# Kernel tuning notes

Hardware: AMD Instinct MI355X
Metric: run time of the kernel (lower is better)

The kernel has to match this reference:

```python
import jax, jax.numpy as jnp
import numpy as np

B, D, S = 16384, 2048, 512      # batch, input_dim, sideinfo_dim
E, H1, H2 = 8, 1024, 512        # subexpert_num, subexpert_unit
EPS = 1e-5                       # BatchNorm eps (torch default)


def setup_inputs() -> dict:
    key = jax.random.key(0)
    ks = jax.random.split(key, 16)
    inp = {
        "input": jax.random.normal(ks[0], (B, D), jnp.float32),
        "sideinfo": jax.random.normal(ks[1], (B, S), jnp.float32),
        # expert layer 1: Linear(D->H1) per expert, batched over E
        "W1": jax.random.normal(ks[2], (E, D, H1), jnp.float32) / np.sqrt(D),
        "b1": jax.random.normal(ks[3], (E, H1), jnp.float32) * 0.01,
        "gamma1": 1.0 + 0.01 * jax.random.normal(ks[4], (E, H1), jnp.float32),
        "beta1": jax.random.normal(ks[5], (E, H1), jnp.float32) * 0.01,
        "mean1": jax.random.normal(ks[6], (E, H1), jnp.float32) * 0.01,
        "var1": jax.random.uniform(ks[7], (E, H1), jnp.float32, 0.5, 1.5),
        # expert layer 2: Linear(H1->H2) per expert
        "W2": jax.random.normal(ks[8], (E, H1, H2), jnp.float32) / np.sqrt(H1),
        "b2": jax.random.normal(ks[9], (E, H2), jnp.float32) * 0.01,
        "gamma2": 1.0 + 0.01 * jax.random.normal(ks[10], (E, H2), jnp.float32),
        "beta2": jax.random.normal(ks[11], (E, H2), jnp.float32) * 0.01,
        "mean2": jax.random.normal(ks[12], (E, H2), jnp.float32) * 0.01,
        "var2": jax.random.uniform(ks[13], (E, H2), jnp.float32, 0.5, 1.5),
        # gate: Linear(S->E) + softmax
        "Wg": jax.random.normal(ks[14], (S, E), jnp.float32) / np.sqrt(S),
        "bg": jax.random.normal(ks[15], (E,), jnp.float32) * 0.01,
    }
    return inp


def _bn(x, gamma, beta, mean, var):
    # eval-mode BatchNorm1d with per-expert running stats; x: [B,E,H]
    return (x - mean) * (gamma * jax.lax.rsqrt(var + EPS)) + beta


def reference(input, sideinfo, W1, b1, gamma1, beta1, mean1, var1,
              W2, b2, gamma2, beta2, mean2, var2, Wg, bg):
    # all E expert MLPs as two batched GEMMs (dropout is identity in eval)
    h = jnp.einsum('bd,edh->beh', input, W1) + b1            # [B,E,H1]
    h = jax.nn.relu(_bn(h, gamma1, beta1, mean1, var1))
    o = jnp.einsum('beh,eho->beo', h, W2) + b2               # [B,E,H2]
    o = jax.nn.relu(_bn(o, gamma2, beta2, mean2, var2))
    gate = jax.nn.softmax(sideinfo @ Wg + bg, axis=1)        # [B,E]
    return jnp.einsum('beo,be->bo', o, gate)                 # [B,H2]
```

## Files before the change

kernel.cpp:

```cpp
#include <hip/hip_runtime.h>
#include <hip/hip_bf16.h>

static constexpr int B_  = 16384;
static constexpr int D_  = 2048;
static constexpr int S_  = 512;
static constexpr int E_  = 8;
static constexpr int H1_ = 1024;
static constexpr int H2_ = 512;
static constexpr float EPS_ = 1e-5f;

typedef __bf16 bf16x8 __attribute__((ext_vector_type(8)));
typedef float  f32x4  __attribute__((ext_vector_type(4)));

static __device__ __forceinline__ unsigned short f2bf(float f) {
    unsigned u = __float_as_uint(f);
    unsigned r = (u + 0x7fffu + ((u >> 16) & 1u)) >> 16;
    return (unsigned short)r;
}


__global__ void cvt_bf16_kernel(const float* __restrict__ in, ushort* __restrict__ out, long n) {
    long i = ((long)blockIdx.x * blockDim.x + threadIdx.x) * 4;
    long stride = (long)gridDim.x * blockDim.x * 4;
    for (; i < n; i += stride) {
        float4 v = *(const float4*)(in + i);
        ushort4 o;
        o.x = f2bf(v.x); o.y = f2bf(v.y); o.z = f2bf(v.z); o.w = f2bf(v.w);
        *(ushort4*)(out + i) = o;
    }
}

__global__ void transpose_cvt_kernel(const float* __restrict__ in, ushort* __restrict__ out,
                                     int R, int C) {
    __shared__ float t[64][65];
    int nbr = R >> 6, nbc = C >> 6;
    int bid = blockIdx.x;
    int e = bid / (nbr * nbc);
    int rem = bid % (nbr * nbc);
    int br = (rem / nbc) << 6, bc = (rem % nbc) << 6;
    const float* ip = in + (size_t)e * R * C;
    ushort* op = out + (size_t)e * R * C;
    int tcol = (threadIdx.x & 15) * 4;
    int trow = threadIdx.x >> 4;
#pragma unroll
    for (int p = 0; p < 4; p++) {
        int r = trow + p * 16;
        float4 v = *(const float4*)(ip + (size_t)(br + r) * C + bc + tcol);
        t[r][tcol + 0] = v.x; t[r][tcol + 1] = v.y; t[r][tcol + 2] = v.z; t[r][tcol + 3] = v.w;
    }
    __syncthreads();
#pragma unroll
    for (int p = 0; p < 4; p++) {
        int c = trow + p * 16;
        ushort4 o;
        o.x = f2bf(t[tcol + 0][c]);
        o.y = f2bf(t[tcol + 1][c]);
        o.z = f2bf(t[tcol + 2][c]);
        o.w = f2bf(t[tcol + 3][c]);
        *(ushort4*)(op + (size_t)(bc + c) * R + br + tcol) = o;
    }
}

__global__ void fold_bn_kernel(const float* __restrict__ gamma, const float* __restrict__ beta,
                               const float* __restrict__ mean, const float* __restrict__ var,
                               const float* __restrict__ bias,
                               float* __restrict__ Sv, float* __restrict__ Tv, int n) {
    int i = blockIdx.x * 256 + threadIdx.x;
    if (i < n) {
        float s = gamma[i] * rsqrtf(var[i] + EPS_);
        Sv[i] = s;
        Tv[i] = (bias[i] - mean[i]) * s + beta[i];
    }
}

__global__ void gate_kernel(const float* __restrict__ side, const float* __restrict__ Wg,
                            const float* __restrict__ bg, float* __restrict__ gate) {
    int wid = threadIdx.x >> 6, lane = threadIdx.x & 63;
    int b = blockIdx.x * 4 + wid;
    const float* sp = side + (size_t)b * S_ + lane * 8;
    float4 v0 = *(const float4*)sp;
    float4 v1 = *(const float4*)(sp + 4);
    float sv[8] = {v0.x, v0.y, v0.z, v0.w, v1.x, v1.y, v1.z, v1.w};
    float acc[E_] = {0,0,0,0,0,0,0,0};
    const float* wrow = Wg + (size_t)(lane * 8) * E_;
#pragma unroll
    for (int j = 0; j < 8; j++) {
        float4 w0 = *(const float4*)(wrow + j * E_);
        float4 w1 = *(const float4*)(wrow + j * E_ + 4);
        acc[0] += sv[j] * w0.x; acc[1] += sv[j] * w0.y;
        acc[2] += sv[j] * w0.z; acc[3] += sv[j] * w0.w;
        acc[4] += sv[j] * w1.x; acc[5] += sv[j] * w1.y;
        acc[6] += sv[j] * w1.z; acc[7] += sv[j] * w1.w;
    }
#pragma unroll
    for (int off = 32; off; off >>= 1)
#pragma unroll
        for (int e = 0; e < E_; e++) acc[e] += __shfl_xor(acc[e], off, 64);
    float m = -1e30f;
#pragma unroll
    for (int e = 0; e < E_; e++) { acc[e] += bg[e]; m = fmaxf(m, acc[e]); }
    float s = 0.f;
#pragma unroll
    for (int e = 0; e < E_; e++) { acc[e] = __expf(acc[e] - m); s += acc[e]; }
    float inv = 1.f / s;
    if (lane < E_) gate[(size_t)b * E_ + lane] = acc[lane] * inv;
}


__device__ __forceinline__ void g2lds16(const void* g, void* l) {
    __builtin_amdgcn_global_load_lds((const __attribute__((address_space(1))) unsigned int*)g,
                                     (__attribute__((address_space(3))) unsigned int*)l,
                                     16, 0, 0);
}

#define BAR()      asm volatile("s_barrier" ::: "memory")
#define WAITVM(n)  asm volatile("s_waitcnt vmcnt(" #n ")" ::: "memory")
#define MFMA(a,b,c) __builtin_amdgcn_mfma_f32_16x16x32_bf16((a),(b),(c),0,0,0)


template<int EPI>
__global__ __launch_bounds__(512, 2)
void gemm8(const ushort* __restrict__ A, const ushort* __restrict__ Bt, long aBatch,
           const float* __restrict__ Sv, const float* __restrict__ Tv,
           ushort* __restrict__ hout, float* __restrict__ outp, const float* __restrict__ gate,
           int M, int N, int K, int tilesN, int tilesM)
{
    extern __shared__ char smem[];

    const int NT  = K >> 6;
    const int tpe = tilesM * tilesN;

    const int nwg = gridDim.x, per = nwg >> 3;
    const int b0  = blockIdx.x;
    const int bid = (b0 & 7) * per + (b0 >> 3);

    const int e   = bid / tpe;
    const int rem = bid % tpe;
    const int tm  = rem / tilesN, tn = rem % tilesN;

    const char* aBase = (const char*)(A + (size_t)e * aBatch + (size_t)tm * 256 * K);
    const char* bBase = (const char*)(Bt + (size_t)e * N * K + (size_t)tn * 256 * K);
    const size_t rowB = (size_t)K * 2;
    const size_t half2 = 64 * rowB;
    const size_t half1 = 128 * rowB;

    const int tid = threadIdx.x, w = tid >> 6, lane = tid & 63;
    const int wm = w >> 2, wn = w & 3;

    const int srow = tid >> 3;
    const int scol_sw = ((tid & 7) * 16) ^ ((srow & 7) << 4);
    const int ldsW = w * 1024;

    const int lr = lane & 15;
    const int cks0 = ((lane >> 4) * 16) ^ ((lane & 7) << 4);
    const int cks1 = (64 + (lane >> 4) * 16) ^ ((lane & 7) << 4);
    const char* rdA0 = smem + 65536 + (wm * 128 + lr) * 128 + cks0;
    const char* rdA1 = smem + 65536 + (wm * 128 + lr) * 128 + cks1;
    const char* rdB0 = smem + (wn * 64 + lr) * 128 + cks0;
    const char* rdB1 = smem + (wn * 64 + lr) * 128 + cks1;

#define STG(gp, ldsoff) do { \
        g2lds16((gp), smem + (ldsoff)); \
        g2lds16((gp) + half2, smem + (ldsoff) + 8192); } while (0)

    const char* ga = aBase + (size_t)srow * rowB + scol_sw;
    const char* gb = bBase + (size_t)srow * rowB + scol_sw;

    f32x4 acc[8][4] = {};
    bf16x8 aC[4], aN[4], bC[4], bN[4];

    STG(ga,         65536 + 0 + 0     + ldsW);
    STG(ga + half1, 65536 + 0 + 16384 + ldsW);
    STG(gb,         0     + 0 + 0     + ldsW);
    STG(gb + half1, 0     + 0 + 16384 + ldsW);
    WAITVM(0);
    BAR();

#pragma unroll
    for (int mf = 0; mf < 4; ++mf) aC[mf] = *(const bf16x8*)(rdA0 + mf * 2048);
#pragma unroll
    for (int nf = 0; nf < 4; ++nf) bC[nf] = *(const bf16x8*)(rdB0 + nf * 2048);

    const char* spA0 = ga + 128;
    const char* spA1 = ga + half1 + 128;
    const char* spB0 = gb + 128;
    const char* spB1 = gb + half1 + 128;

#pragma unroll 2
    for (int t = 0; t < NT; ++t) {
        const int bi   = t & 1;
        const int oR   = bi * 32768;
        const int oRN  = (bi ^ 1) * 32768;
        const int oSA  = 65536 + (bi ^ 1) * 32768;
        const int oSB  = (bi ^ 1) * 32768;
        const bool more = (t < NT - 1);

#pragma unroll
        for (int mf = 0; mf < 4; ++mf) aN[mf] = *(const bf16x8*)(rdA0 + oR + (4 + mf) * 2048);
        if (more) {
            STG(spA0, oSA + 0 + ldsW);
            STG(spA1, oSA + 16384 + ldsW);
        }
        __builtin_amdgcn_s_setprio(1);
#pragma unroll
        for (int mf = 0; mf < 4; ++mf)
#pragma unroll
            for (int nf = 0; nf < 4; ++nf)
                acc[mf][nf] = MFMA(aC[mf], bC[nf], acc[mf][nf]);
        __builtin_amdgcn_s_setprio(0);

#pragma unroll
        for (int mf = 0; mf < 4; ++mf) aC[mf] = *(const bf16x8*)(rdA1 + oR + mf * 2048);
#pragma unroll
        for (int nf = 0; nf < 4; ++nf) bN[nf] = *(const bf16x8*)(rdB1 + oR + nf * 2048);
        if (more) STG(spB0, oSB + 0 + ldsW);
        __builtin_amdgcn_s_setprio(1);
#pragma unroll
        for (int mf = 0; mf < 4; ++mf)
#pragma unroll
            for (int nf = 0; nf < 4; ++nf)
                acc[4 + mf][nf] = MFMA(aN[mf], bC[nf], acc[4 + mf][nf]);
        __builtin_amdgcn_s_setprio(0);

#pragma unroll
        for (int mf = 0; mf < 4; ++mf) aN[mf] = *(const bf16x8*)(rdA1 + oR + (4 + mf) * 2048);
        if (more) STG(spB1, oSB + 16384 + ldsW);
        __builtin_amdgcn_s_setprio(1);
#pragma unroll
        for (int mf = 0; mf < 4; ++mf)
#pragma unroll
            for (int nf = 0; nf < 4; ++nf)
                acc[mf][nf] = MFMA(aC[mf], bN[nf], acc[mf][nf]);
        __builtin_amdgcn_s_setprio(0);

        __builtin_amdgcn_s_setprio(1);
#pragma unroll
        for (int mf = 0; mf < 4; ++mf)
#pragma unroll
            for (int nf = 0; nf < 4; ++nf)
                acc[4 + mf][nf] = MFMA(aN[mf], bN[nf], acc[4 + mf][nf]);
        __builtin_amdgcn_s_setprio(0);

        if (more) {
            WAITVM(0);
            BAR();
#pragma unroll
            for (int mf = 0; mf < 4; ++mf) aC[mf] = *(const bf16x8*)(rdA0 + oRN + mf * 2048);
#pragma unroll
            for (int nf = 0; nf < 4; ++nf) bC[nf] = *(const bf16x8*)(rdB0 + oRN + nf * 2048);
        }

        spA0 += 128; spA1 += 128; spB0 += 128; spB1 += 128;
    }

    const int rbase = tm * 256 + wm * 128 + (lane >> 4) * 4;
    const int cbase = tn * 256 + wn * 64 + lr;
    if (EPI == 1) {
#pragma unroll
        for (int nf = 0; nf < 4; ++nf) {
            const int col = cbase + nf * 16;
            const float s = Sv[e * N + col];
            const float tt = Tv[e * N + col];
#pragma unroll
            for (int mf = 0; mf < 8; ++mf) {
                const int row0 = rbase + mf * 16;
                f32x4 v = acc[mf][nf];
#pragma unroll
                for (int r = 0; r < 4; ++r) {
                    float x = v[r] * s + tt;
                    x = x > 0.f ? x : 0.f;
                    hout[((size_t)e * M + row0 + r) * N + col] = f2bf(x);
                }
            }
        }
    }
#undef STG
}


__global__ __launch_bounds__(512, 2)
void gemm2e(const ushort* __restrict__ H, const ushort* __restrict__ W2T,
            const float* __restrict__ Sv, const float* __restrict__ Tv,
            const float* __restrict__ gate, float* __restrict__ outp)
{
    extern __shared__ char smem[];

    const int b0 = blockIdx.x;
    const int bid = (b0 & 7) * 32 + (b0 >> 3);
    const int tm = bid >> 1, tn = bid & 1;

    const size_t rowB  = (size_t)H1_ * 2;
    const size_t strAE = (size_t)B_ * H1_ * 2;
    const size_t strBE = (size_t)H2_ * H1_ * 2;
    const size_t half2 = 64 * rowB;
    const size_t halfB = 128 * rowB;

    const int tid = threadIdx.x, w = tid >> 6, lane = tid & 63;
    const int wm = w >> 2, wn = w & 3;

    const int srow = tid >> 3;
    const int scol_sw = ((tid & 7) * 16) ^ ((srow & 7) << 4);
    const int ldsW = w * 1024;

    const int lr = lane & 15;
    const int cks0 = ((lane >> 4) * 16) ^ ((lane & 7) << 4);
    const int cks1 = (64 + (lane >> 4) * 16) ^ ((lane & 7) << 4);
    const char* rdA0 = smem + 65536 + (wm * 64 + lr) * 128 + cks0;
    const char* rdA1 = smem + 65536 + (wm * 64 + lr) * 128 + cks1;
    const char* rdB0 = smem + (wn * 64 + lr) * 128 + cks0;
    const char* rdB1 = smem + (wn * 64 + lr) * 128 + cks1;

    const char* ga = (const char*)H + (size_t)tm * 128 * rowB + (size_t)srow * rowB + scol_sw;
    const char* gb = (const char*)W2T + (size_t)tn * 256 * rowB + (size_t)srow * rowB + scol_sw;

    f32x4 acc[4][4] = {};
    f32x4 oacc[4][4] = {};
    bf16x8 a0[4], a1[4], b0v[4], b1v[4];

    g2lds16(ga,                 smem + 65536 + 0     + ldsW);
    g2lds16(ga + half2,         smem + 65536 + 8192  + ldsW);
    g2lds16(gb,                 smem + 0     + ldsW);
    g2lds16(gb + half2,         smem + 8192  + ldsW);
    g2lds16(gb + halfB,         smem + 16384 + ldsW);
    g2lds16(gb + halfB + half2, smem + 24576 + ldsW);
    WAITVM(0);
    BAR();

#pragma unroll
    for (int mf = 0; mf < 4; ++mf) a0[mf] = *(const bf16x8*)(rdA0 + mf * 2048);
#pragma unroll
    for (int nf = 0; nf < 4; ++nf) b0v[nf] = *(const bf16x8*)(rdB0 + nf * 2048);

    const int rbase = tm * 128 + wm * 64 + (lane >> 4) * 4;
    const int cbase = tn * 256 + wn * 64 + lr;

#pragma unroll 2
    for (int t = 0; t < 128; ++t) {
        const int bi   = t & 1;
        const int oA   = bi * 16384;
        const int oB   = bi * 32768;
        const int oAn  = (bi ^ 1) * 16384;
        const int oBn  = (bi ^ 1) * 32768;
        const bool more = (t < 127);

        const int t1 = t + 1;
        const char* gA1 = ga + (size_t)(t1 >> 4) * strAE + (t1 & 15) * 128;
        const char* gB1 = gb + (size_t)(t1 >> 4) * strBE + (t1 & 15) * 128;

#pragma unroll
        for (int mf = 0; mf < 4; ++mf) a1[mf] = *(const bf16x8*)(rdA1 + oA + mf * 2048);
#pragma unroll
        for (int nf = 0; nf < 4; ++nf) b1v[nf] = *(const bf16x8*)(rdB1 + oB + nf * 2048);
        if (more) {
            g2lds16(gA1,         smem + 65536 + oAn + 0    + ldsW);
            g2lds16(gA1 + half2, smem + 65536 + oAn + 8192 + ldsW);
            g2lds16(gB1,         smem + oBn + 0    + ldsW);
            g2lds16(gB1 + half2, smem + oBn + 8192 + ldsW);
        }
        __builtin_amdgcn_s_setprio(1);
#pragma unroll
        for (int mf = 0; mf < 4; ++mf)
#pragma unroll
            for (int nf = 0; nf < 4; ++nf)
                acc[mf][nf] = MFMA(a0[mf], b0v[nf], acc[mf][nf]);
        __builtin_amdgcn_s_setprio(0);

        if (more) {
            g2lds16(gB1 + halfB,         smem + oBn + 16384 + ldsW);
            g2lds16(gB1 + halfB + half2, smem + oBn + 24576 + ldsW);
        }
        __builtin_amdgcn_s_setprio(1);
#pragma unroll
        for (int mf = 0; mf < 4; ++mf)
#pragma unroll
            for (int nf = 0; nf < 4; ++nf)
                acc[mf][nf] = MFMA(a1[mf], b1v[nf], acc[mf][nf]);
        __builtin_amdgcn_s_setprio(0);

        if (more) {
            WAITVM(0);
            BAR();
#pragma unroll
            for (int mf = 0; mf < 4; ++mf) a0[mf] = *(const bf16x8*)(rdA0 + oAn + mf * 2048);
#pragma unroll
            for (int nf = 0; nf < 4; ++nf) b0v[nf] = *(const bf16x8*)(rdB0 + oBn + nf * 2048);
        }

        if ((t & 15) == 15) {
            const int e = t >> 4;
            float sc[4], tc[4];
#pragma unroll
            for (int nf = 0; nf < 4; ++nf) {
                sc[nf] = Sv[e * H2_ + cbase + nf * 16];
                tc[nf] = Tv[e * H2_ + cbase + nf * 16];
            }
#pragma unroll
            for (int mf = 0; mf < 4; ++mf) {
#pragma unroll
                for (int r = 0; r < 4; ++r) {
                    const int row = rbase + mf * 16 + r;
                    const float g = gate[(size_t)row * E_ + e];
#pragma unroll
                    for (int nf = 0; nf < 4; ++nf) {
                        float x = acc[mf][nf][r] * sc[nf] + tc[nf];
                        x = x > 0.f ? x : 0.f;
                        oacc[mf][nf][r] += g * x;
                    }
                }
            }
#pragma unroll
            for (int mf = 0; mf < 4; ++mf)
#pragma unroll
                for (int nf = 0; nf < 4; ++nf)
                    acc[mf][nf] = (f32x4){0.f, 0.f, 0.f, 0.f};
        }
    }

#pragma unroll
    for (int mf = 0; mf < 4; ++mf) {
#pragma unroll
        for (int r = 0; r < 4; ++r) {
            const int row = rbase + mf * 16 + r;
#pragma unroll
            for (int nf = 0; nf < 4; ++nf)
                outp[(size_t)row * H2_ + cbase + nf * 16] = oacc[mf][nf][r];
        }
    }
}


extern "C" void kernel_launch(void* const* d_in, const int* in_sizes, int n_in,
                              void* d_out, int out_size, void* d_ws, size_t ws_size,
                              hipStream_t stream) {
    (void)in_sizes; (void)n_in; (void)out_size; (void)ws_size;

    const float* input    = (const float*)d_in[0];
    const float* sideinfo = (const float*)d_in[1];
    const float* W1   = (const float*)d_in[2];
    const float* b1   = (const float*)d_in[3];
    const float* g1   = (const float*)d_in[4];
    const float* be1  = (const float*)d_in[5];
    const float* m1   = (const float*)d_in[6];
    const float* v1   = (const float*)d_in[7];
    const float* W2   = (const float*)d_in[8];
    const float* b2   = (const float*)d_in[9];
    const float* g2   = (const float*)d_in[10];
    const float* be2  = (const float*)d_in[11];
    const float* m2   = (const float*)d_in[12];
    const float* v2   = (const float*)d_in[13];
    const float* Wg   = (const float*)d_in[14];
    const float* bg   = (const float*)d_in[15];

    char* w = (char*)d_ws;
    size_t off = 0;
    auto carve = [&](size_t bytes) {
        void* p = w + off;
        off += (bytes + 255) & ~(size_t)255;
        return p;
    };
    ushort* Abf  = (ushort*)carve((size_t)B_ * D_ * 2);
    ushort* W1T  = (ushort*)carve((size_t)E_ * H1_ * D_ * 2);
    ushort* W2T  = (ushort*)carve((size_t)E_ * H2_ * H1_ * 2);
    ushort* hbuf = (ushort*)carve((size_t)E_ * B_ * H1_ * 2);
    float*  S1   = (float*)carve((size_t)E_ * H1_ * 4);
    float*  T1   = (float*)carve((size_t)E_ * H1_ * 4);
    float*  S2   = (float*)carve((size_t)E_ * H2_ * 4);
    float*  T2   = (float*)carve((size_t)E_ * H2_ * 4);
    float*  gatep = (float*)carve((size_t)B_ * E_ * 4);

    float* outp = (float*)d_out;

    hipFuncSetAttribute(reinterpret_cast<const void*>(&gemm8<1>),
                        hipFuncAttributeMaxDynamicSharedMemorySize, 131072);
    hipFuncSetAttribute(reinterpret_cast<const void*>(&gemm2e),
                        hipFuncAttributeMaxDynamicSharedMemorySize, 98304);

    cvt_bf16_kernel<<<4096, 256, 0, stream>>>(input, Abf, (long)B_ * D_);
    transpose_cvt_kernel<<<E_ * (D_ / 64) * (H1_ / 64), 256, 0, stream>>>(W1, W1T, D_, H1_);
    transpose_cvt_kernel<<<E_ * (H1_ / 64) * (H2_ / 64), 256, 0, stream>>>(W2, W2T, H1_, H2_);
    fold_bn_kernel<<<(E_ * H1_ + 255) / 256, 256, 0, stream>>>(g1, be1, m1, v1, b1, S1, T1, E_ * H1_);
    fold_bn_kernel<<<(E_ * H2_ + 255) / 256, 256, 0, stream>>>(g2, be2, m2, v2, b2, S2, T2, E_ * H2_);
    gate_kernel<<<B_ / 4, 256, 0, stream>>>(sideinfo, Wg, bg, gatep);

    gemm8<1><<<E_ * (B_ / 256) * (H1_ / 256), 512, 131072, stream>>>(
        Abf, W1T, 0L, S1, T1, hbuf, nullptr, nullptr, B_, H1_, D_, H1_ / 256, B_ / 256);

    gemm2e<<<(B_ / 128) * (H2_ / 256), 512, 98304, stream>>>(
        hbuf, W2T, S2, T2, gatep, outp);
}
```

Measured before the change: 803.2 us.

## Triple-buffer LDS staging in second-layer GEMM for two-deep prefetch

The second-layer expert GEMM goes from double-buffered to triple-buffered LDS staging. Global-to-LDS loads for k-step t+2 are issued while step t computes, and the wait only needs the older batch to land (vmcnt 6), so memory latency gets more slack. The cost is LDS growing from 96KB to 144KB per block, which still fits in the 160KB LDS of MI355X at one block per CU, and the loop is no longer unrolled by 2.

Result: faster. 742.8 us (-7.5%).

```diff
diff --git a/kernel.cpp b/kernel.cpp
--- a/kernel.cpp
+++ b/kernel.cpp
@@ -305,58 +305,55 @@
     const int lr = lane & 15;
     const int cks0 = ((lane >> 4) * 16) ^ ((lane & 7) << 4);
     const int cks1 = (64 + (lane >> 4) * 16) ^ ((lane & 7) << 4);
-    const char* rdA0 = smem + 65536 + (wm * 64 + lr) * 128 + cks0;
-    const char* rdA1 = smem + 65536 + (wm * 64 + lr) * 128 + cks1;
+    const char* rdA0 = smem + (wm * 64 + lr) * 128 + cks0;
+    const char* rdA1 = smem + (wm * 64 + lr) * 128 + cks1;
     const char* rdB0 = smem + (wn * 64 + lr) * 128 + cks0;
     const char* rdB1 = smem + (wn * 64 + lr) * 128 + cks1;
 
     const char* ga = (const char*)H + (size_t)tm * 128 * rowB + (size_t)srow * rowB + scol_sw;
     const char* gb = (const char*)W2T + (size_t)tn * 256 * rowB + (size_t)srow * rowB + scol_sw;
+
+#define STG6(gAp, gBp, aOff, bOff) do { \
+        g2lds16((gAp),                 smem + (aOff) + 0     + ldsW); \
+        g2lds16((gAp) + half2,         smem + (aOff) + 8192  + ldsW); \
+        g2lds16((gBp),                 smem + (bOff) + 0     + ldsW); \
+        g2lds16((gBp) + half2,         smem + (bOff) + 8192  + ldsW); \
+        g2lds16((gBp) + halfB,         smem + (bOff) + 16384 + ldsW); \
+        g2lds16((gBp) + halfB + half2, smem + (bOff) + 24576 + ldsW); } while (0)
 
     f32x4 acc[4][4] = {};
     f32x4 oacc[4][4] = {};
     bf16x8 a0[4], a1[4], b0v[4], b1v[4];
 
-    g2lds16(ga,                 smem + 65536 + 0     + ldsW);
-    g2lds16(ga + half2,         smem + 65536 + 8192  + ldsW);
-    g2lds16(gb,                 smem + 0     + ldsW);
-    g2lds16(gb + half2,         smem + 8192  + ldsW);
-    g2lds16(gb + halfB,         smem + 16384 + ldsW);
-    g2lds16(gb + halfB + half2, smem + 24576 + ldsW);
-    WAITVM(0);
+    int aCur = 98304, aN1 = 114688, aN2 = 131072;
+    int bCur = 0,     bN1 = 32768,  bN2 = 65536;
+
+    STG6(ga, gb, aCur, bCur);
+    STG6(ga + 128, gb + 128, aN1, bN1);
+    WAITVM(6);
     BAR();
 
 #pragma unroll
-    for (int mf = 0; mf < 4; ++mf) a0[mf] = *(const bf16x8*)(rdA0 + mf * 2048);
-#pragma unroll
-    for (int nf = 0; nf < 4; ++nf) b0v[nf] = *(const bf16x8*)(rdB0 + nf * 2048);
+    for (int mf = 0; mf < 4; ++mf) a0[mf] = *(const bf16x8*)(rdA0 + aCur + mf * 2048);
+#pragma unroll
+    for (int nf = 0; nf < 4; ++nf) b0v[nf] = *(const bf16x8*)(rdB0 + bCur + nf * 2048);
 
     const int rbase = tm * 128 + wm * 64 + (lane >> 4) * 4;
     const int cbase = tn * 256 + wn * 64 + lr;
 
-#pragma unroll 2
     for (int t = 0; t < 128; ++t) {
-        const int bi   = t & 1;
-        const int oA   = bi * 16384;
-        const int oB   = bi * 32768;
-        const int oAn  = (bi ^ 1) * 16384;
-        const int oBn  = (bi ^ 1) * 32768;
-        const bool more = (t < 127);
-
-        const int t1 = t + 1;
-        const char* gA1 = ga + (size_t)(t1 >> 4) * strAE + (t1 & 15) * 128;
-        const char* gB1 = gb + (size_t)(t1 >> 4) * strBE + (t1 & 15) * 128;
-
-#pragma unroll
-        for (int mf = 0; mf < 4; ++mf) a1[mf] = *(const bf16x8*)(rdA1 + oA + mf * 2048);
-#pragma unroll
-        for (int nf = 0; nf < 4; ++nf) b1v[nf] = *(const bf16x8*)(rdB1 + oB + nf * 2048);
-        if (more) {
-            g2lds16(gA1,         smem + 65536 + oAn + 0    + ldsW);
-            g2lds16(gA1 + half2, smem + 65536 + oAn + 8192 + ldsW);
-            g2lds16(gB1,         smem + oBn + 0    + ldsW);
-            g2lds16(gB1 + half2, smem + oBn + 8192 + ldsW);
-        }
+        const int t2 = t + 2;
+        const bool moreS = (t2 < 128);
+        const bool moreT = (t < 127);
+
+        const char* gA2 = ga + (size_t)(t2 >> 4) * strAE + (t2 & 15) * 128;
+        const char* gB2 = gb + (size_t)(t2 >> 4) * strBE + (t2 & 15) * 128;
+
+#pragma unroll
+        for (int mf = 0; mf < 4; ++mf) a1[mf] = *(const bf16x8*)(rdA1 + aCur + mf * 2048);
+#pragma unroll
+        for (int nf = 0; nf < 4; ++nf) b1v[nf] = *(const bf16x8*)(rdB1 + bCur + nf * 2048);
+        if (moreS) STG6(gA2, gB2, aN2, bN2);
         __builtin_amdgcn_s_setprio(1);
 #pragma unroll
         for (int mf = 0; mf < 4; ++mf)
@@ -365,10 +362,6 @@
                 acc[mf][nf] = MFMA(a0[mf], b0v[nf], acc[mf][nf]);
         __builtin_amdgcn_s_setprio(0);
 
-        if (more) {
-            g2lds16(gB1 + halfB,         smem + oBn + 16384 + ldsW);
-            g2lds16(gB1 + halfB + half2, smem + oBn + 24576 + ldsW);
-        }
         __builtin_amdgcn_s_setprio(1);
 #pragma unroll
         for (int mf = 0; mf < 4; ++mf)
@@ -377,13 +370,13 @@
                 acc[mf][nf] = MFMA(a1[mf], b1v[nf], acc[mf][nf]);
         __builtin_amdgcn_s_setprio(0);
 
-        if (more) {
-            WAITVM(0);
+        if (moreT) {
+            if (moreS) { WAITVM(6); } else { WAITVM(0); }
             BAR();
 #pragma unroll
-            for (int mf = 0; mf < 4; ++mf) a0[mf] = *(const bf16x8*)(rdA0 + oAn + mf * 2048);
-#pragma unroll
-            for (int nf = 0; nf < 4; ++nf) b0v[nf] = *(const bf16x8*)(rdB0 + oBn + nf * 2048);
+            for (int mf = 0; mf < 4; ++mf) a0[mf] = *(const bf16x8*)(rdA0 + aN1 + mf * 2048);
+#pragma unroll
+            for (int nf = 0; nf < 4; ++nf) b0v[nf] = *(const bf16x8*)(rdB0 + bN1 + nf * 2048);
         }
 
         if ((t & 15) == 15) {
@@ -414,6 +407,9 @@
                 for (int nf = 0; nf < 4; ++nf)
                     acc[mf][nf] = (f32x4){0.f, 0.f, 0.f, 0.f};
         }
+
+        const int ta = aCur; aCur = aN1; aN1 = aN2; aN2 = ta;
+        const int tb = bCur; bCur = bN1; bN1 = bN2; bN2 = tb;
     }
 
 #pragma unroll
@@ -426,6 +422,7 @@
                 outp[(size_t)row * H2_ + cbase + nf * 16] = oacc[mf][nf][r];
         }
     }
+#undef STG6
 }
 
 
@@ -473,7 +470,7 @@
     hipFuncSetAttribute(reinterpret_cast<const void*>(&gemm8<1>),
                         hipFuncAttributeMaxDynamicSharedMemorySize, 131072);
     hipFuncSetAttribute(reinterpret_cast<const void*>(&gemm2e),
-                        hipFuncAttributeMaxDynamicSharedMemorySize, 98304);
+                        hipFuncAttributeMaxDynamicSharedMemorySize, 147456);
 
     cvt_bf16_kernel<<<4096, 256, 0, stream>>>(input, Abf, (long)B_ * D_);
     transpose_cvt_kernel<<<E_ * (D_ / 64) * (H1_ / 64), 256, 0, stream>>>(W1, W1T, D_, H1_);
@@ -485,6 +482,6 @@
     gemm8<1><<<E_ * (B_ / 256) * (H1_ / 256), 512, 131072, stream>>>(
         Abf, W1T, 0L, S1, T1, hbuf, nullptr, nullptr, B_, H1_, D_, H1_ / 256, B_ / 256);
 
-    gemm2e<<<(B_ / 128) * (H2_ / 256), 512, 98304, stream>>>(
+    gemm2e<<<(B_ / 128) * (H2_ / 256), 512, 147456, stream>>>(
         hbuf, W2T, S2, T2, gatep, outp);
 }
```
